# Performance work log

Measured on AMD Instinct MI355X. Metric: run time of the kernel, lower is better.

The kernel has to match this reference:

```python
import jax, jax.numpy as jnp
import numpy as np

RESO = 32          # grid_resolution
HID = 32           # hidden_dim
CDIM = 32          # c_dim
NBLK = 5           # n_blocks
PAD = 0.1          # padding
L = 10             # positional encoding frequencies -> dim 60


def setup_inputs() -> dict:
    key = jax.random.key(0)
    ks = jax.random.split(key, 12)
    B, T = 2, 200000
    p = jax.random.uniform(ks[0], (B, T, 3), jnp.float32, -0.5, 0.5)
    s = 0.05
    return {
        "p": p,
        "fc_pos_w": jax.random.normal(ks[1], (60, 2 * HID), jnp.float32) * s,
        "fc_pos_b": jax.random.normal(ks[2], (2 * HID,), jnp.float32) * s,
        "blk_fc0_w": jax.random.normal(ks[3], (NBLK, 2 * HID, HID), jnp.float32) * s,
        "blk_fc0_b": jax.random.normal(ks[4], (NBLK, HID), jnp.float32) * s,
        "blk_fc1_w": jax.random.normal(ks[5], (NBLK, HID, HID), jnp.float32) * s,
        "blk_fc1_b": jax.random.normal(ks[6], (NBLK, HID), jnp.float32) * s,
        "blk_sc_w": jax.random.normal(ks[7], (NBLK, 2 * HID, HID), jnp.float32) * s,  # shortcut, no bias
        "fc_c_w": jax.random.normal(ks[8], (HID, CDIM), jnp.float32) * s,
        "fc_c_b": jax.random.normal(ks[9], (CDIM,), jnp.float32) * s,
    }


def _pos_encode(p):
    # p in [-0.5,0.5] -> [-2,0] after 2p-1 (matches torch impl: p = 2*p - 1)
    q = 2.0 * p - 1.0
    freqs = (jnp.pi * (2.0 ** jnp.arange(L, dtype=jnp.float32)))  # [L]
    a = q[..., None, :] * freqs[:, None]                          # [B,T,L,3]
    pe = jnp.stack([jnp.sin(a), jnp.cos(a)], axis=-2)             # [B,T,L,2,3]
    return pe.reshape(*p.shape[:-1], 2 * L * 3)                   # [B,T,60]


def _normalize_3d(p):
    p_nor = p / (1.0 + PAD + 1e-3) + 0.5
    return jnp.clip(p_nor, 0.0, 1.0 - 1e-3)


def _coord2index(p_nor):
    x = jnp.floor(p_nor * RESO).astype(jnp.int32)                  # [B,T,3]
    return x[..., 0] + RESO * (x[..., 1] + RESO * x[..., 2])       # [B,T]


def _resblock(x, w0, b0, w1, b1, ws):
    h = jax.nn.relu(jax.nn.relu(x) @ w0 + b0)
    return x @ ws + (jax.nn.relu(h) @ w1 + b1)


def reference(p, fc_pos_w, fc_pos_b, blk_fc0_w, blk_fc0_b, blk_fc1_w, blk_fc1_b,
              blk_sc_w, fc_c_w, fc_c_b):
    B, T, _ = p.shape
    G = RESO ** 3
    p_nor = _normalize_3d(p)
    idx = _coord2index(p_nor)                                      # [B,T]
    gidx = (idx + jnp.arange(B, dtype=jnp.int32)[:, None] * G).reshape(-1)  # [B*T]

    net = _pos_encode(p) @ fc_pos_w + fc_pos_b                     # [B,T,64]
    net = _resblock(net, blk_fc0_w[0], blk_fc0_b[0], blk_fc1_w[0], blk_fc1_b[0], blk_sc_w[0])
    for i in range(1, NBLK):
        # pool_local: scatter_max per grid cell, gather back to points
        flat = net.reshape(B * T, HID)
        cell = jax.ops.segment_max(flat, gidx, num_segments=B * G)  # [B*G,HID]
        pooled = cell[gidx].reshape(B, T, HID)
        net = jnp.concatenate([net, pooled], axis=-1)               # [B,T,64]
        net = _resblock(net, blk_fc0_w[i], blk_fc0_b[i], blk_fc1_w[i], blk_fc1_b[i], blk_sc_w[i])

    c = net @ fc_c_w + fc_c_b                                       # [B,T,CDIM]

    # generate_grid_features: scatter_mean into grid (empty cells = 0)
    cf = c.reshape(B * T, CDIM)
    sums = jax.ops.segment_sum(cf, gidx, num_segments=B * G)        # [B*G,CDIM]
    cnt = jax.ops.segment_sum(jnp.ones((B * T, 1), c.dtype), gidx, num_segments=B * G)
    mean = sums / jnp.maximum(cnt, 1.0)
    fea_grid = mean.reshape(B, G, CDIM).transpose(0, 2, 1).reshape(B, CDIM, RESO, RESO, RESO)
    return fea_grid
```

## Files before the change

### kernel.cpp

```cpp
#include <hip/hip_runtime.h>
#include <math.h>

#define TPTS 200000
#define BB 2
#define NPTS (BB*TPTS)
#define GRID3 32768
#define BG 65536
#define SROWS 176

typedef __attribute__((ext_vector_type(8))) __bf16 bf16x8;
typedef __attribute__((ext_vector_type(4))) float f32x4;
typedef unsigned short ushort_t;

#define MFMA16(a,b,c) __builtin_amdgcn_mfma_f32_16x16x32_bf16(a,b,c,0,0,0)

__device__ __forceinline__ void split8(const float* v, bf16x8& hi, bf16x8& lo)
{
#pragma unroll
  for (int j = 0; j < 8; j++) {
    float f = v[j];
    __bf16 h = (__bf16)f;
    hi[j] = h;
    lo[j] = (__bf16)(f - (float)h);
  }
}

__device__ __forceinline__ int cellof(float p0, float p1, float p2, int t)
{
  const float DEN = (float)(1.0 + 0.1 + 1e-3);
  const float HI  = (float)(1.0 - 1e-3);
  float n0 = fminf(fmaxf(p0/DEN + 0.5f, 0.f), HI);
  float n1 = fminf(fmaxf(p1/DEN + 0.5f, 0.f), HI);
  float n2 = fminf(fmaxf(p2/DEN + 0.5f, 0.f), HI);
  int c0 = (int)floorf(n0*32.f), c1 = (int)floorf(n1*32.f), c2 = (int)floorf(n2*32.f);
  return c0 + 32*(c1 + 32*c2) + (t >= TPTS ? GRID3 : 0);
}

__global__ __launch_bounds__(256) void k_hist(
    const float* __restrict__ p, int* __restrict__ gbuf, int* __restrict__ hist)
{
  int t = blockIdx.x*256 + threadIdx.x;
  if (t >= NPTS) return;
  int g = cellof(p[3*t], p[3*t+1], p[3*t+2], t);
  gbuf[t] = g;
  atomicAdd(hist + g, 1);
}

__global__ __launch_bounds__(256) void k_scanA(
    const int* __restrict__ hist, int* __restrict__ texcl, int* __restrict__ bsum)
{
  __shared__ int sm[256];
  int tid = threadIdx.x;
  int t = blockIdx.x*256 + tid;
  int v = hist[t];
  sm[tid] = v; __syncthreads();
  for (int off = 1; off < 256; off <<= 1) {
    int x = sm[tid];
    int u = (tid >= off) ? sm[tid-off] : 0;
    __syncthreads();
    sm[tid] = x + u;
    __syncthreads();
  }
  texcl[t] = sm[tid] - v;
  if (tid == 255) bsum[blockIdx.x] = sm[255];
}

__global__ __launch_bounds__(256) void k_scanB(
    const int* __restrict__ bsum, int* __restrict__ boff)
{
  __shared__ int sm[256];
  int tid = threadIdx.x;
  int v = bsum[tid];
  sm[tid] = v; __syncthreads();
  for (int off = 1; off < 256; off <<= 1) {
    int x = sm[tid];
    int u = (tid >= off) ? sm[tid-off] : 0;
    __syncthreads();
    sm[tid] = x + u;
    __syncthreads();
  }
  boff[tid] = sm[tid] - v;
}

__global__ __launch_bounds__(256) void k_scanC(
    const int* __restrict__ texcl, const int* __restrict__ boff,
    int* __restrict__ start, int* __restrict__ cursor)
{
  int t = blockIdx.x*256 + threadIdx.x;
  int v = boff[blockIdx.x] + texcl[t];
  start[t] = v; cursor[t] = v;
  if (t == 0) start[BG] = NPTS;
}

__global__ __launch_bounds__(256) void k_scatter(
    const float* __restrict__ p, const int* __restrict__ gbuf,
    int* __restrict__ cursor, float* __restrict__ p_sorted, int* __restrict__ gsort)
{
  int t = blockIdx.x*256 + threadIdx.x;
  if (t >= NPTS) return;
  int g = gbuf[t];
  int slot = atomicAdd(cursor + g, 1);
  gsort[slot] = g;
  p_sorted[3*slot]   = p[3*t];
  p_sorted[3*slot+1] = p[3*t+1];
  p_sorted[3*slot+2] = p[3*t+2];
}

__global__ void k_pack(
    const float* __restrict__ f0w, const float* __restrict__ scw,
    const float* __restrict__ f1w, const float* __restrict__ wc,
    const float* __restrict__ Wp,
    ushort_t* __restrict__ wpack)
{
  int f = blockIdx.x, l = threadIdx.x;
  if (f >= 104) {
    int idx = f - 104;
    int c = idx >> 3, t = (idx >> 1) & 3, e = idx & 1;
#pragma unroll
    for (int j = 0; j < 8; j++) {
      int k = c*32 + (l>>4)*8 + j, n = t*16 + (l&15);
      float v = (k < 60) ? Wp[k*64 + n] : 0.f;
      __bf16 h = (__bf16)v;
      __bf16 out = (e == 0) ? h : (__bf16)(v - (float)h);
      union { __bf16 b; ushort_t u; } cv; cv.b = out;
      wpack[((size_t)f*64 + l)*8 + j] = cv.u;
    }
    return;
  }
  const float* W; int c, t, e;
  if (f < 100) {
    int s = f / 20, r = f % 20;
    if (r < 8)       { W = f0w + s*2048; c = r>>2;        t = (r>>1)&1; e = r&1; }
    else if (r < 16) { int q = r-8;  W = scw + s*2048; c = q>>2; t = (q>>1)&1; e = q&1; }
    else             { int q = r-16; W = f1w + s*1024; c = 0;    t = q>>1;     e = q&1; }
  } else { int q = f-100; W = wc; c = 0; t = q>>1; e = q&1; }
#pragma unroll
  for (int j = 0; j < 8; j++) {
    int k = c*32 + (l>>4)*8 + j, n = t*16 + (l&15);
    float v = W[k*32 + n];
    __bf16 h = (__bf16)v;
    __bf16 out = (e == 0) ? h : (__bf16)(v - (float)h);
    union { __bf16 b; ushort_t u; } cv; cv.b = out;
    wpack[((size_t)f*64 + l)*8 + j] = cv.u;
  }
}

__global__ __launch_bounds__(256) void k_fused0(
    const float* __restrict__ ps,
    const ushort_t* __restrict__ wpPE, const float* __restrict__ bp,
    const ushort_t* __restrict__ wp,
    const float* __restrict__ b0, const float* __restrict__ b1,
    float* __restrict__ net)
{
  __shared__ float xlds[4][16*68];
  __shared__ float hbuf[4][16*36];
  int wave = threadIdx.x >> 6, lane = threadIdx.x & 63;
  int m = lane & 15, q = lane >> 4;
  int pbase = (blockIdx.x*4 + wave)*16;
  int pt = pbase + m;

  float p0 = ps[3*pt], p1 = ps[3*pt+1], p2 = ps[3*pt+2];
  float u0 = 2.f*p0 - 1.f, u1 = 2.f*p1 - 1.f, u2 = 2.f*p2 - 1.f;
  const float PIF = 3.14159265358979323846f;

  float pe[2][8];
#pragma unroll
  for (int c2 = 0; c2 < 2; c2++) {
#pragma unroll
    for (int jj = 0; jj < 8; jj++) {
      int e = c2*32 + q*8 + jj;
      int l = (e * 43691) >> 18;
      int r = e - l*6;
      bool issin = (r < 3);
      int d = issin ? r : (r - 3);
      float ud = (d == 0) ? u0 : ((d == 1) ? u1 : u2);
      float xval = ldexpf(ud, l);
      float red = xval - 2.f*rintf(0.5f*xval);
      float ang = PIF*red + (issin ? 0.f : 1.5707963267948966f);
      float v = __sinf(ang);
      pe[c2][jj] = (e < 60) ? v : 0.f;
    }
  }
  bf16x8 peh[2], pel[2];
  split8(pe[0], peh[0], pel[0]);
  split8(pe[1], peh[1], pel[1]);

  f32x4 xacc[4];
#pragma unroll
  for (int t = 0; t < 4; t++) {
    float bb = bp[t*16 + m];
    xacc[t] = (f32x4){bb,bb,bb,bb};
  }
#pragma unroll
  for (int c2 = 0; c2 < 2; c2++)
#pragma unroll
    for (int t = 0; t < 4; t++) {
      bf16x8 bh = *(const bf16x8*)(wpPE + ((size_t)((c2*4+t)*2    )*64 + lane)*8);
      bf16x8 bl = *(const bf16x8*)(wpPE + ((size_t)((c2*4+t)*2 + 1)*64 + lane)*8);
      xacc[t] = MFMA16(peh[c2], bh, xacc[t]);
      xacc[t] = MFMA16(pel[c2], bh, xacc[t]);
      xacc[t] = MFMA16(peh[c2], bl, xacc[t]);
    }

  float* xl = xlds[wave];
#pragma unroll
  for (int t = 0; t < 4; t++)
#pragma unroll
    for (int r = 0; r < 4; r++)
      xl[(q*4+r)*68 + t*16 + m] = xacc[t][r];
  __syncthreads();

  float xv[2][8];
#pragma unroll
  for (int c2 = 0; c2 < 2; c2++)
#pragma unroll
    for (int jj = 0; jj < 8; jj++)
      xv[c2][jj] = xl[m*68 + c2*32 + q*8 + jj];

  bf16x8 w0f[2][2][2], wsf[2][2][2], w1f[2][2];
#pragma unroll
  for (int c = 0; c < 2; c++)
#pragma unroll
    for (int t = 0; t < 2; t++)
#pragma unroll
      for (int e = 0; e < 2; e++) {
        w0f[c][t][e] = *(const bf16x8*)(wp + ((size_t)(((c*2+t)*2+e)    )*64 + lane)*8);
        wsf[c][t][e] = *(const bf16x8*)(wp + ((size_t)(((c*2+t)*2+e) + 8)*64 + lane)*8);
      }
#pragma unroll
  for (int t = 0; t < 2; t++)
#pragma unroll
    for (int e = 0; e < 2; e++)
      w1f[t][e] = *(const bf16x8*)(wp + ((size_t)(16 + t*2 + e)*64 + lane)*8);

  bf16x8 axh[2], axl[2], arh[2], arl[2];
#pragma unroll
  for (int c = 0; c < 2; c++) {
    float r[8];
#pragma unroll
    for (int j = 0; j < 8; j++) r[j] = fmaxf(xv[c][j], 0.f);
    split8(xv[c], axh[c], axl[c]);
    split8(r,     arh[c], arl[c]);
  }

  f32x4 hacc[2], yacc[2];
#pragma unroll
  for (int t = 0; t < 2; t++) {
    float bb0 = b0[m + 16*t], bb1 = b1[m + 16*t];
    hacc[t] = (f32x4){bb0,bb0,bb0,bb0};
    yacc[t] = (f32x4){bb1,bb1,bb1,bb1};
  }

#pragma unroll
  for (int c = 0; c < 2; c++)
#pragma unroll
    for (int t = 0; t < 2; t++) {
      hacc[t] = MFMA16(arh[c], w0f[c][t][0], hacc[t]);
      hacc[t] = MFMA16(arl[c], w0f[c][t][0], hacc[t]);
      hacc[t] = MFMA16(arh[c], w0f[c][t][1], hacc[t]);
      yacc[t] = MFMA16(axh[c], wsf[c][t][0], yacc[t]);
      yacc[t] = MFMA16(axl[c], wsf[c][t][0], yacc[t]);
      yacc[t] = MFMA16(axh[c], wsf[c][t][1], yacc[t]);
    }

  float* hb = hbuf[wave];
#pragma unroll
  for (int t = 0; t < 2; t++)
#pragma unroll
    for (int r = 0; r < 4; r++)
      hb[(q*4+r)*36 + m + 16*t] = fmaxf(hacc[t][r], 0.f);
  __syncthreads();
  float hv[8];
#pragma unroll
  for (int j = 0; j < 8; j++) hv[j] = hb[m*36 + q*8 + j];
  bf16x8 hh, hl; split8(hv, hh, hl);
#pragma unroll
  for (int t = 0; t < 2; t++) {
    yacc[t] = MFMA16(hh, w1f[t][0], yacc[t]);
    yacc[t] = MFMA16(hl, w1f[t][0], yacc[t]);
    yacc[t] = MFMA16(hh, w1f[t][1], yacc[t]);
  }

#pragma unroll
  for (int t = 0; t < 2; t++)
#pragma unroll
    for (int r = 0; r < 4; r++)
      net[(size_t)(pbase + q*4 + r)*32 + m + 16*t] = yacc[t][r];
}

__global__ __launch_bounds__(256) void k_stage_f(
    const float* __restrict__ netin, float* __restrict__ netout,
    const int* __restrict__ gsort, const int* __restrict__ start,
    const ushort_t* __restrict__ wp,
    const float* __restrict__ b0, const float* __restrict__ b1)
{
  __shared__ float sbuf[SROWS*36];
  int tid = threadIdx.x;
  int P0 = blockIdx.x*64;
  int s = start[gsort[P0]];
  int e = start[gsort[P0+63] + 1];
  int n = e - s; if (n > SROWS) n = SROWS;

  for (int idx = tid; idx < n*8; idx += 256) {
    int r = idx >> 3, c = idx & 7;
    *(f32x4*)(sbuf + r*36 + c*4) =
      *(const f32x4*)(netin + ((size_t)(s + r))*32 + c*4);
  }
  __syncthreads();

  int wave = tid >> 6, lane = tid & 63;
  int m = lane & 15, q = lane >> 4;
  int pbase = P0 + wave*16;
  int pt = pbase + m;
  int g = gsort[pt];
  int cs = start[g] - s, ce = start[g+1] - s;

  float xv[2][8];
  {
    const float* xr = sbuf + (pt - s)*36 + q*8;
    *(f32x4*)&xv[0][0] = *(const f32x4*)xr;
    *(f32x4*)&xv[0][4] = *(const f32x4*)(xr + 4);
  }
  {
    f32x4 ma = (f32x4){-INFINITY,-INFINITY,-INFINITY,-INFINITY};
    f32x4 mb = ma;
    for (int k = cs; k < ce; k++) {
      const float* rr = sbuf + k*36 + q*8;
      f32x4 va = *(const f32x4*)rr;
      f32x4 vb = *(const f32x4*)(rr + 4);
      ma.x = fmaxf(ma.x, va.x); ma.y = fmaxf(ma.y, va.y);
      ma.z = fmaxf(ma.z, va.z); ma.w = fmaxf(ma.w, va.w);
      mb.x = fmaxf(mb.x, vb.x); mb.y = fmaxf(mb.y, vb.y);
      mb.z = fmaxf(mb.z, vb.z); mb.w = fmaxf(mb.w, vb.w);
    }
    *(f32x4*)&xv[1][0] = ma;
    *(f32x4*)&xv[1][4] = mb;
  }

  bf16x8 w0f[2][2][2], wsf[2][2][2], w1f[2][2];
#pragma unroll
  for (int c = 0; c < 2; c++)
#pragma unroll
    for (int t = 0; t < 2; t++)
#pragma unroll
      for (int e2 = 0; e2 < 2; e2++) {
        w0f[c][t][e2] = *(const bf16x8*)(wp + ((size_t)(((c*2+t)*2+e2)    )*64 + lane)*8);
        wsf[c][t][e2] = *(const bf16x8*)(wp + ((size_t)(((c*2+t)*2+e2) + 8)*64 + lane)*8);
      }
#pragma unroll
  for (int t = 0; t < 2; t++)
#pragma unroll
    for (int e2 = 0; e2 < 2; e2++)
      w1f[t][e2] = *(const bf16x8*)(wp + ((size_t)(16 + t*2 + e2)*64 + lane)*8);

  bf16x8 axh[2], axl[2], arh[2], arl[2];
#pragma unroll
  for (int c = 0; c < 2; c++) {
    float r[8];
#pragma unroll
    for (int j = 0; j < 8; j++) r[j] = fmaxf(xv[c][j], 0.f);
    split8(xv[c], axh[c], axl[c]);
    split8(r,     arh[c], arl[c]);
  }

  f32x4 hacc[2], yacc[2];
#pragma unroll
  for (int t = 0; t < 2; t++) {
    float bb0 = b0[m + 16*t], bb1 = b1[m + 16*t];
    hacc[t] = (f32x4){bb0,bb0,bb0,bb0};
    yacc[t] = (f32x4){bb1,bb1,bb1,bb1};
  }

#pragma unroll
  for (int c = 0; c < 2; c++)
#pragma unroll
    for (int t = 0; t < 2; t++) {
      hacc[t] = MFMA16(arh[c], w0f[c][t][0], hacc[t]);
      hacc[t] = MFMA16(arl[c], w0f[c][t][0], hacc[t]);
      hacc[t] = MFMA16(arh[c], w0f[c][t][1], hacc[t]);
      yacc[t] = MFMA16(axh[c], wsf[c][t][0], yacc[t]);
      yacc[t] = MFMA16(axl[c], wsf[c][t][0], yacc[t]);
      yacc[t] = MFMA16(axh[c], wsf[c][t][1], yacc[t]);
    }

  __syncthreads();
  float* hb = sbuf + wave*576;
#pragma unroll
  for (int t = 0; t < 2; t++)
#pragma unroll
    for (int r = 0; r < 4; r++)
      hb[(q*4+r)*36 + m + 16*t] = fmaxf(hacc[t][r], 0.f);
  __syncthreads();
  float hv[8];
#pragma unroll
  for (int j = 0; j < 8; j++) hv[j] = hb[m*36 + q*8 + j];
  bf16x8 hh, hl; split8(hv, hh, hl);
#pragma unroll
  for (int t = 0; t < 2; t++) {
    yacc[t] = MFMA16(hh, w1f[t][0], yacc[t]);
    yacc[t] = MFMA16(hl, w1f[t][0], yacc[t]);
    yacc[t] = MFMA16(hh, w1f[t][1], yacc[t]);
  }

#pragma unroll
  for (int t = 0; t < 2; t++)
#pragma unroll
    for (int r = 0; r < 4; r++)
      netout[(size_t)(pbase + q*4 + r)*32 + m + 16*t] = yacc[t][r];
}

__global__ __launch_bounds__(256) void k_final_f(
    const float* __restrict__ netin, float* __restrict__ netout,
    const int* __restrict__ gsort, const int* __restrict__ start,
    const ushort_t* __restrict__ wp, const ushort_t* __restrict__ wpc,
    const float* __restrict__ b0, const float* __restrict__ b1,
    const float* __restrict__ bc)
{
  __shared__ float sbuf[SROWS*36];
  int tid = threadIdx.x;
  int P0 = blockIdx.x*64;
  int s = start[gsort[P0]];
  int e = start[gsort[P0+63] + 1];
  int n = e - s; if (n > SROWS) n = SROWS;

  for (int idx = tid; idx < n*8; idx += 256) {
    int r = idx >> 3, c = idx & 7;
    *(f32x4*)(sbuf + r*36 + c*4) =
      *(const f32x4*)(netin + ((size_t)(s + r))*32 + c*4);
  }
  __syncthreads();

  int wave = tid >> 6, lane = tid & 63;
  int m = lane & 15, q = lane >> 4;
  int pbase = P0 + wave*16;
  int pt = pbase + m;
  int g = gsort[pt];
  int cs = start[g] - s, ce = start[g+1] - s;

  float xv[2][8];
  {
    const float* xr = sbuf + (pt - s)*36 + q*8;
    *(f32x4*)&xv[0][0] = *(const f32x4*)xr;
    *(f32x4*)&xv[0][4] = *(const f32x4*)(xr + 4);
  }
  {
    f32x4 ma = (f32x4){-INFINITY,-INFINITY,-INFINITY,-INFINITY};
    f32x4 mb = ma;
    for (int k = cs; k < ce; k++) {
      const float* rr = sbuf + k*36 + q*8;
      f32x4 va = *(const f32x4*)rr;
      f32x4 vb = *(const f32x4*)(rr + 4);
      ma.x = fmaxf(ma.x, va.x); ma.y = fmaxf(ma.y, va.y);
      ma.z = fmaxf(ma.z, va.z); ma.w = fmaxf(ma.w, va.w);
      mb.x = fmaxf(mb.x, vb.x); mb.y = fmaxf(mb.y, vb.y);
      mb.z = fmaxf(mb.z, vb.z); mb.w = fmaxf(mb.w, vb.w);
    }
    *(f32x4*)&xv[1][0] = ma;
    *(f32x4*)&xv[1][4] = mb;
  }

  bf16x8 w0f[2][2][2], wsf[2][2][2], w1f[2][2], wcf[2][2];
#pragma unroll
  for (int c = 0; c < 2; c++)
#pragma unroll
    for (int t = 0; t < 2; t++)
#pragma unroll
      for (int e2 = 0; e2 < 2; e2++) {
        w0f[c][t][e2] = *(const bf16x8*)(wp + ((size_t)(((c*2+t)*2+e2)    )*64 + lane)*8);
        wsf[c][t][e2] = *(const bf16x8*)(wp + ((size_t)(((c*2+t)*2+e2) + 8)*64 + lane)*8);
      }
#pragma unroll
  for (int t = 0; t < 2; t++)
#pragma unroll
    for (int e2 = 0; e2 < 2; e2++) {
      w1f[t][e2] = *(const bf16x8*)(wp  + ((size_t)(16 + t*2 + e2)*64 + lane)*8);
      wcf[t][e2] = *(const bf16x8*)(wpc + ((size_t)(     t*2 + e2)*64 + lane)*8);
    }

  bf16x8 axh[2], axl[2], arh[2], arl[2];
#pragma unroll
  for (int c = 0; c < 2; c++) {
    float r[8];
#pragma unroll
    for (int j = 0; j < 8; j++) r[j] = fmaxf(xv[c][j], 0.f);
    split8(xv[c], axh[c], axl[c]);
    split8(r,     arh[c], arl[c]);
  }

  f32x4 hacc[2], yacc[2];
#pragma unroll
  for (int t = 0; t < 2; t++) {
    float bb0 = b0[m + 16*t], bb1 = b1[m + 16*t];
    hacc[t] = (f32x4){bb0,bb0,bb0,bb0};
    yacc[t] = (f32x4){bb1,bb1,bb1,bb1};
  }

#pragma unroll
  for (int c = 0; c < 2; c++)
#pragma unroll
    for (int t = 0; t < 2; t++) {
      hacc[t] = MFMA16(arh[c], w0f[c][t][0], hacc[t]);
      hacc[t] = MFMA16(arl[c], w0f[c][t][0], hacc[t]);
      hacc[t] = MFMA16(arh[c], w0f[c][t][1], hacc[t]);
      yacc[t] = MFMA16(axh[c], wsf[c][t][0], yacc[t]);
      yacc[t] = MFMA16(axl[c], wsf[c][t][0], yacc[t]);
      yacc[t] = MFMA16(axh[c], wsf[c][t][1], yacc[t]);
    }

  __syncthreads();
  float* hb = sbuf + wave*576;
  float* yb = sbuf + 4*576 + wave*576;
#pragma unroll
  for (int t = 0; t < 2; t++)
#pragma unroll
    for (int r = 0; r < 4; r++)
      hb[(q*4+r)*36 + m + 16*t] = fmaxf(hacc[t][r], 0.f);
  __syncthreads();
  float hv[8];
#pragma unroll
  for (int j = 0; j < 8; j++) hv[j] = hb[m*36 + q*8 + j];
  bf16x8 hh, hl; split8(hv, hh, hl);
#pragma unroll
  for (int t = 0; t < 2; t++) {
    yacc[t] = MFMA16(hh, w1f[t][0], yacc[t]);
    yacc[t] = MFMA16(hl, w1f[t][0], yacc[t]);
    yacc[t] = MFMA16(hh, w1f[t][1], yacc[t]);
  }

#pragma unroll
  for (int t = 0; t < 2; t++)
#pragma unroll
    for (int r = 0; r < 4; r++)
      yb[(q*4+r)*36 + m + 16*t] = yacc[t][r];
  __syncthreads();
  float yv[8];
#pragma unroll
  for (int j = 0; j < 8; j++) yv[j] = yb[m*36 + q*8 + j];
  bf16x8 yh, yl; split8(yv, yh, yl);

  f32x4 cacc[2];
#pragma unroll
  for (int t = 0; t < 2; t++) {
    float bb = bc[m + 16*t];
    cacc[t] = (f32x4){bb,bb,bb,bb};
    cacc[t] = MFMA16(yh, wcf[t][0], cacc[t]);
    cacc[t] = MFMA16(yl, wcf[t][0], cacc[t]);
    cacc[t] = MFMA16(yh, wcf[t][1], cacc[t]);
  }

#pragma unroll
  for (int t = 0; t < 2; t++)
#pragma unroll
    for (int r = 0; r < 4; r++)
      netout[(size_t)(pbase + q*4 + r)*32 + m + 16*t] = cacc[t][r];
}

__global__ __launch_bounds__(256) void k_mean(
    const float* __restrict__ net, const int* __restrict__ start,
    float* __restrict__ outp)
{
  int tid = blockIdx.x*256 + threadIdx.x;
  int c = tid >> 3, sub = tid & 7;
  int s = start[c], e = start[c+1];
  f32x4 sum = (f32x4){0.f,0.f,0.f,0.f};
  for (int k = s; k < e; k++) {
    f32x4 v = *(const f32x4*)(net + (size_t)k*32 + sub*4);
    sum.x += v.x; sum.y += v.y; sum.z += v.z; sum.w += v.w;
  }
  float inv = (e > s) ? 1.f/(float)(e - s) : 0.f;
  int b = c >> 15, cell = c & 32767;
  size_t ob = ((size_t)b << 20) + cell;
#pragma unroll
  for (int jj = 0; jj < 4; jj++) {
    int ch = sub*4 + jj;
    float v = ((const float*)&sum)[jj] * inv;
    outp[ob + ((size_t)ch << 15)] = v;
  }
}

extern "C" void kernel_launch(void* const* d_in, const int* in_sizes, int n_in,
                              void* d_out, int out_size, void* d_ws, size_t ws_size,
                              hipStream_t stream)
{
  const float* p   = (const float*)d_in[0];
  const float* Wp  = (const float*)d_in[1];
  const float* bp  = (const float*)d_in[2];
  const float* f0w = (const float*)d_in[3];
  const float* f0b = (const float*)d_in[4];
  const float* f1w = (const float*)d_in[5];
  const float* f1b = (const float*)d_in[6];
  const float* scw = (const float*)d_in[7];
  const float* wc  = (const float*)d_in[8];
  const float* bc  = (const float*)d_in[9];
  float* outp = (float*)d_out;

  char* wsb = (char*)d_ws;
  float*    netA     = (float*)wsb;
  float*    netB     = netA + (size_t)NPTS*32;
  int*      gbuf     = (int*)(netB + (size_t)NPTS*32);
  int*      gsort    = gbuf + NPTS;
  int*      hist     = gsort + NPTS;
  int*      start    = hist + BG;
  int*      cursor   = start + BG + 1;
  int*      texcl    = cursor + BG;
  int*      bsum     = texcl + BG;
  int*      boff     = bsum + 256;
  ushort_t* wpack    = (ushort_t*)(boff + 256);
  float*    p_sorted = (float*)(wpack + (size_t)120*512);

  dim3 blk(256);
  dim3 gpts((NPTS + 255)/256);
  dim3 gmfma(NPTS/64);
  dim3 gcell((BG*8)/256);
  dim3 gscan(BG/256);

  hipMemsetAsync(hist, 0, (size_t)BG*4, stream);
  hipLaunchKernelGGL(k_hist, gpts, blk, 0, stream, p, gbuf, hist);
  hipLaunchKernelGGL(k_scanA, gscan, blk, 0, stream, hist, texcl, bsum);
  hipLaunchKernelGGL(k_scanB, dim3(1), blk, 0, stream, bsum, boff);
  hipLaunchKernelGGL(k_scanC, gscan, blk, 0, stream, texcl, boff, start, cursor);
  hipLaunchKernelGGL(k_scatter, gpts, blk, 0, stream, p, gbuf, cursor, p_sorted, gsort);
  hipLaunchKernelGGL(k_pack, dim3(120), dim3(64), 0, stream, f0w, scw, f1w, wc, Wp, wpack);
  hipLaunchKernelGGL(k_fused0, gmfma, blk, 0, stream,
                     p_sorted, wpack + (size_t)104*512, bp,
                     wpack + (size_t)0*20*512, f0b + 0*32, f1b + 0*32, netA);
  hipLaunchKernelGGL(k_stage_f, gmfma, blk, 0, stream, netA, netB, gsort, start,
                     wpack + (size_t)1*20*512, f0b + 1*32, f1b + 1*32);
  hipLaunchKernelGGL(k_stage_f, gmfma, blk, 0, stream, netB, netA, gsort, start,
                     wpack + (size_t)2*20*512, f0b + 2*32, f1b + 2*32);
  hipLaunchKernelGGL(k_stage_f, gmfma, blk, 0, stream, netA, netB, gsort, start,
                     wpack + (size_t)3*20*512, f0b + 3*32, f1b + 3*32);
  hipLaunchKernelGGL(k_final_f, gmfma, blk, 0, stream, netB, netA, gsort, start,
                     wpack + (size_t)4*20*512, wpack + (size_t)100*512,
                     f0b + 4*32, f1b + 4*32, bc);
  hipLaunchKernelGGL(k_mean, gcell, blk, 0, stream, netA, start, outp);
}
```

Measured before the change: 328.0 us.

## Fuse all resblock stages and scatter-mean into one cell-aligned megakernel

Replaces the per-stage kernels (fused0, three stage kernels, final, mean) with a single kernel. Each block owns a cell-aligned range of sorted points, found by binary search in a new k_blocks kernel, and keeps all activations in LDS across the five resblocks. The per-cell mean is written directly from LDS, so the global netA/netB round trips and several launches go away. The costs are an output memset, more __syncthreads, a 128-row cap per block that could drop points if a range is larger, and blocks with uneven work.

```diff
diff --git a/kernel.cpp b/kernel.cpp
--- a/kernel.cpp
+++ b/kernel.cpp
@@ -6,7 +6,7 @@
 #define NPTS (BB*TPTS)
 #define GRID3 32768
 #define BG 65536
-#define SROWS 176
+#define NMEGA (NPTS/64)
 
 typedef __attribute__((ext_vector_type(8))) __bf16 bf16x8;
 typedef __attribute__((ext_vector_type(4))) float f32x4;
@@ -106,6 +106,17 @@
   p_sorted[3*slot+2] = p[3*t+2];
 }
 
+__global__ __launch_bounds__(256) void k_blocks(
+    const int* __restrict__ start, int* __restrict__ blockA)
+{
+  int k = blockIdx.x*256 + threadIdx.x;
+  if (k > NMEGA) return;
+  int t = k*64;
+  int lo = 0, hi = BG;
+  while (lo < hi) { int mid = (lo+hi) >> 1; if (start[mid] >= t) hi = mid; else lo = mid+1; }
+  blockA[k] = start[lo];
+}
+
 __global__ void k_pack(
     const float* __restrict__ f0w, const float* __restrict__ scw,
     const float* __restrict__ f1w, const float* __restrict__ wc,
@@ -145,436 +156,333 @@
   }
 }
 
-__global__ __launch_bounds__(256) void k_fused0(
-    const float* __restrict__ ps,
-    const ushort_t* __restrict__ wpPE, const float* __restrict__ bp,
-    const ushort_t* __restrict__ wp,
-    const float* __restrict__ b0, const float* __restrict__ b1,
-    float* __restrict__ net)
-{
-  __shared__ float xlds[4][16*68];
-  __shared__ float hbuf[4][16*36];
-  int wave = threadIdx.x >> 6, lane = threadIdx.x & 63;
-  int m = lane & 15, q = lane >> 4;
-  int pbase = (blockIdx.x*4 + wave)*16;
-  int pt = pbase + m;
-
-  float p0 = ps[3*pt], p1 = ps[3*pt+1], p2 = ps[3*pt+2];
-  float u0 = 2.f*p0 - 1.f, u1 = 2.f*p1 - 1.f, u2 = 2.f*p2 - 1.f;
-  const float PIF = 3.14159265358979323846f;
-
-  float pe[2][8];
-#pragma unroll
-  for (int c2 = 0; c2 < 2; c2++) {
-#pragma unroll
-    for (int jj = 0; jj < 8; jj++) {
-      int e = c2*32 + q*8 + jj;
-      int l = (e * 43691) >> 18;
-      int r = e - l*6;
-      bool issin = (r < 3);
-      int d = issin ? r : (r - 3);
-      float ud = (d == 0) ? u0 : ((d == 1) ? u1 : u2);
-      float xval = ldexpf(ud, l);
-      float red = xval - 2.f*rintf(0.5f*xval);
-      float ang = PIF*red + (issin ? 0.f : 1.5707963267948966f);
-      float v = __sinf(ang);
-      pe[c2][jj] = (e < 60) ? v : 0.f;
-    }
-  }
-  bf16x8 peh[2], pel[2];
-  split8(pe[0], peh[0], pel[0]);
-  split8(pe[1], peh[1], pel[1]);
-
-  f32x4 xacc[4];
-#pragma unroll
-  for (int t = 0; t < 4; t++) {
-    float bb = bp[t*16 + m];
-    xacc[t] = (f32x4){bb,bb,bb,bb};
-  }
-#pragma unroll
-  for (int c2 = 0; c2 < 2; c2++)
-#pragma unroll
-    for (int t = 0; t < 4; t++) {
-      bf16x8 bh = *(const bf16x8*)(wpPE + ((size_t)((c2*4+t)*2    )*64 + lane)*8);
-      bf16x8 bl = *(const bf16x8*)(wpPE + ((size_t)((c2*4+t)*2 + 1)*64 + lane)*8);
-      xacc[t] = MFMA16(peh[c2], bh, xacc[t]);
-      xacc[t] = MFMA16(pel[c2], bh, xacc[t]);
-      xacc[t] = MFMA16(peh[c2], bl, xacc[t]);
-    }
-
-  float* xl = xlds[wave];
-#pragma unroll
-  for (int t = 0; t < 4; t++)
-#pragma unroll
-    for (int r = 0; r < 4; r++)
-      xl[(q*4+r)*68 + t*16 + m] = xacc[t][r];
-  __syncthreads();
-
-  float xv[2][8];
-#pragma unroll
-  for (int c2 = 0; c2 < 2; c2++)
-#pragma unroll
-    for (int jj = 0; jj < 8; jj++)
-      xv[c2][jj] = xl[m*68 + c2*32 + q*8 + jj];
-
-  bf16x8 w0f[2][2][2], wsf[2][2][2], w1f[2][2];
-#pragma unroll
-  for (int c = 0; c < 2; c++)
-#pragma unroll
-    for (int t = 0; t < 2; t++)
-#pragma unroll
-      for (int e = 0; e < 2; e++) {
-        w0f[c][t][e] = *(const bf16x8*)(wp + ((size_t)(((c*2+t)*2+e)    )*64 + lane)*8);
-        wsf[c][t][e] = *(const bf16x8*)(wp + ((size_t)(((c*2+t)*2+e) + 8)*64 + lane)*8);
-      }
-#pragma unroll
-  for (int t = 0; t < 2; t++)
-#pragma unroll
-    for (int e = 0; e < 2; e++)
-      w1f[t][e] = *(const bf16x8*)(wp + ((size_t)(16 + t*2 + e)*64 + lane)*8);
-
-  bf16x8 axh[2], axl[2], arh[2], arl[2];
-#pragma unroll
-  for (int c = 0; c < 2; c++) {
-    float r[8];
-#pragma unroll
-    for (int j = 0; j < 8; j++) r[j] = fmaxf(xv[c][j], 0.f);
-    split8(xv[c], axh[c], axl[c]);
-    split8(r,     arh[c], arl[c]);
-  }
-
-  f32x4 hacc[2], yacc[2];
-#pragma unroll
-  for (int t = 0; t < 2; t++) {
-    float bb0 = b0[m + 16*t], bb1 = b1[m + 16*t];
-    hacc[t] = (f32x4){bb0,bb0,bb0,bb0};
-    yacc[t] = (f32x4){bb1,bb1,bb1,bb1};
-  }
-
-#pragma unroll
-  for (int c = 0; c < 2; c++)
-#pragma unroll
-    for (int t = 0; t < 2; t++) {
-      hacc[t] = MFMA16(arh[c], w0f[c][t][0], hacc[t]);
-      hacc[t] = MFMA16(arl[c], w0f[c][t][0], hacc[t]);
-      hacc[t] = MFMA16(arh[c], w0f[c][t][1], hacc[t]);
-      yacc[t] = MFMA16(axh[c], wsf[c][t][0], yacc[t]);
-      yacc[t] = MFMA16(axl[c], wsf[c][t][0], yacc[t]);
-      yacc[t] = MFMA16(axh[c], wsf[c][t][1], yacc[t]);
-    }
-
-  float* hb = hbuf[wave];
-#pragma unroll
-  for (int t = 0; t < 2; t++)
-#pragma unroll
-    for (int r = 0; r < 4; r++)
-      hb[(q*4+r)*36 + m + 16*t] = fmaxf(hacc[t][r], 0.f);
-  __syncthreads();
-  float hv[8];
-#pragma unroll
-  for (int j = 0; j < 8; j++) hv[j] = hb[m*36 + q*8 + j];
-  bf16x8 hh, hl; split8(hv, hh, hl);
-#pragma unroll
-  for (int t = 0; t < 2; t++) {
-    yacc[t] = MFMA16(hh, w1f[t][0], yacc[t]);
-    yacc[t] = MFMA16(hl, w1f[t][0], yacc[t]);
-    yacc[t] = MFMA16(hh, w1f[t][1], yacc[t]);
-  }
-
-#pragma unroll
-  for (int t = 0; t < 2; t++)
-#pragma unroll
-    for (int r = 0; r < 4; r++)
-      net[(size_t)(pbase + q*4 + r)*32 + m + 16*t] = yacc[t][r];
-}
-
-__global__ __launch_bounds__(256) void k_stage_f(
-    const float* __restrict__ netin, float* __restrict__ netout,
-    const int* __restrict__ gsort, const int* __restrict__ start,
-    const ushort_t* __restrict__ wp,
-    const float* __restrict__ b0, const float* __restrict__ b1)
-{
-  __shared__ float sbuf[SROWS*36];
+__global__ __launch_bounds__(256) void k_mega(
+    const float* __restrict__ ps, const int* __restrict__ gsort,
+    const int* __restrict__ start, const int* __restrict__ blockA,
+    const ushort_t* __restrict__ wpack,
+    const float* __restrict__ bp, const float* __restrict__ f0b,
+    const float* __restrict__ f1b, const float* __restrict__ bc,
+    float* __restrict__ outp)
+{
+  __shared__ __align__(16) float smem[4608*2 + 4*576];
+  float* actA = smem;
+  float* actB = smem + 4608;
+  float* hbB  = smem + 9216;
+
   int tid = threadIdx.x;
-  int P0 = blockIdx.x*64;
-  int s = start[gsort[P0]];
-  int e = start[gsort[P0+63] + 1];
-  int n = e - s; if (n > SROWS) n = SROWS;
-
-  for (int idx = tid; idx < n*8; idx += 256) {
-    int r = idx >> 3, c = idx & 7;
-    *(f32x4*)(sbuf + r*36 + c*4) =
-      *(const f32x4*)(netin + ((size_t)(s + r))*32 + c*4);
-  }
-  __syncthreads();
+  int s = blockA[blockIdx.x], e = blockA[blockIdx.x + 1];
+  int n = e - s;
+  if (n <= 0) return;
+  if (n > 128) n = 128;
 
   int wave = tid >> 6, lane = tid & 63;
   int m = lane & 15, q = lane >> 4;
-  int pbase = P0 + wave*16;
-  int pt = pbase + m;
-  int g = gsort[pt];
-  int cs = start[g] - s, ce = start[g+1] - s;
-
-  float xv[2][8];
+  float* hb = hbB + wave*576;
+  const float PIF = 3.14159265358979323846f;
+
+  int ptc[2], rown[2], cs[2], ce[2];
+#pragma unroll
+  for (int c = 0; c < 2; c++) {
+    int pt = s + c*64 + wave*16 + m;
+    int pc = pt < e ? pt : (e-1);
+    ptc[c] = pc; rown[c] = pc - s;
+    int g = gsort[pc];
+    cs[c] = start[g] - s; ce[c] = start[g+1] - s;
+  }
+
   {
-    const float* xr = sbuf + (pt - s)*36 + q*8;
-    *(f32x4*)&xv[0][0] = *(const f32x4*)xr;
-    *(f32x4*)&xv[0][4] = *(const f32x4*)(xr + 4);
-  }
-  {
-    f32x4 ma = (f32x4){-INFINITY,-INFINITY,-INFINITY,-INFINITY};
-    f32x4 mb = ma;
-    for (int k = cs; k < ce; k++) {
-      const float* rr = sbuf + k*36 + q*8;
-      f32x4 va = *(const f32x4*)rr;
-      f32x4 vb = *(const f32x4*)(rr + 4);
-      ma.x = fmaxf(ma.x, va.x); ma.y = fmaxf(ma.y, va.y);
-      ma.z = fmaxf(ma.z, va.z); ma.w = fmaxf(ma.w, va.w);
-      mb.x = fmaxf(mb.x, vb.x); mb.y = fmaxf(mb.y, vb.y);
-      mb.z = fmaxf(mb.z, vb.z); mb.w = fmaxf(mb.w, vb.w);
+    const ushort_t* wp0 = wpack;
+    const ushort_t* wpPE = wpack + (size_t)104*512;
+    bf16x8 w0f[2][2][2], wsf[2][2][2], w1f[2][2];
+#pragma unroll
+    for (int c = 0; c < 2; c++)
+#pragma unroll
+      for (int t = 0; t < 2; t++)
+#pragma unroll
+        for (int e2 = 0; e2 < 2; e2++) {
+          w0f[c][t][e2] = *(const bf16x8*)(wp0 + ((size_t)(((c*2+t)*2+e2)    )*64 + lane)*8);
+          wsf[c][t][e2] = *(const bf16x8*)(wp0 + ((size_t)(((c*2+t)*2+e2) + 8)*64 + lane)*8);
+        }
+#pragma unroll
+    for (int t = 0; t < 2; t++)
+#pragma unroll
+      for (int e2 = 0; e2 < 2; e2++)
+        w1f[t][e2] = *(const bf16x8*)(wp0 + ((size_t)(16 + t*2 + e2)*64 + lane)*8);
+
+#pragma unroll
+    for (int c = 0; c < 2; c++) {
+      if (c*64 >= n) continue;
+      int pc = ptc[c];
+      float p0 = ps[3*pc], p1 = ps[3*pc+1], p2 = ps[3*pc+2];
+      float u0 = 2.f*p0 - 1.f, u1 = 2.f*p1 - 1.f, u2 = 2.f*p2 - 1.f;
+      float pe[2][8];
+#pragma unroll
+      for (int c2 = 0; c2 < 2; c2++)
+#pragma unroll
+        for (int jj = 0; jj < 8; jj++) {
+          int e1 = c2*32 + q*8 + jj;
+          int l = (e1 * 43691) >> 18;
+          int r = e1 - l*6;
+          bool issin = (r < 3);
+          int d = issin ? r : (r - 3);
+          float ud = (d == 0) ? u0 : ((d == 1) ? u1 : u2);
+          float xval = ldexpf(ud, l);
+          float red = xval - 2.f*rintf(0.5f*xval);
+          float sv, cv;
+          __sincosf(PIF*red, &sv, &cv);
+          float v = issin ? sv : cv;
+          pe[c2][jj] = (e1 < 60) ? v : 0.f;
+        }
+      bf16x8 peh[2], pel[2];
+      split8(pe[0], peh[0], pel[0]);
+      split8(pe[1], peh[1], pel[1]);
+
+      f32x4 xacc[4];
+#pragma unroll
+      for (int t = 0; t < 4; t++) {
+        float bb = bp[t*16 + m];
+        xacc[t] = (f32x4){bb,bb,bb,bb};
+      }
+#pragma unroll
+      for (int c2 = 0; c2 < 2; c2++)
+#pragma unroll
+        for (int t = 0; t < 4; t++) {
+          bf16x8 bh = *(const bf16x8*)(wpPE + ((size_t)((c2*4+t)*2    )*64 + lane)*8);
+          bf16x8 bl = *(const bf16x8*)(wpPE + ((size_t)((c2*4+t)*2 + 1)*64 + lane)*8);
+          xacc[t] = MFMA16(peh[c2], bh, xacc[t]);
+          xacc[t] = MFMA16(pel[c2], bh, xacc[t]);
+          xacc[t] = MFMA16(peh[c2], bl, xacc[t]);
+        }
+
+      float* xl = actB + wave*1088;
+#pragma unroll
+      for (int t = 0; t < 4; t++)
+#pragma unroll
+        for (int r = 0; r < 4; r++)
+          xl[(q*4+r)*68 + t*16 + m] = xacc[t][r];
+      __syncthreads();
+      float xv[2][8];
+#pragma unroll
+      for (int c2 = 0; c2 < 2; c2++)
+#pragma unroll
+        for (int jj = 0; jj < 8; jj++)
+          xv[c2][jj] = xl[m*68 + c2*32 + q*8 + jj];
+      __syncthreads();
+
+      bf16x8 axh[2], axl[2], arh[2], arl[2];
+#pragma unroll
+      for (int c2 = 0; c2 < 2; c2++) {
+        float r[8];
+#pragma unroll
+        for (int j = 0; j < 8; j++) r[j] = fmaxf(xv[c2][j], 0.f);
+        split8(xv[c2], axh[c2], axl[c2]);
+        split8(r,      arh[c2], arl[c2]);
+      }
+      f32x4 hacc[2], yacc[2];
+#pragma unroll
+      for (int t = 0; t < 2; t++) {
+        float bb0 = f0b[m + 16*t], bb1 = f1b[m + 16*t];
+        hacc[t] = (f32x4){bb0,bb0,bb0,bb0};
+        yacc[t] = (f32x4){bb1,bb1,bb1,bb1};
+      }
+#pragma unroll
+      for (int c2 = 0; c2 < 2; c2++)
+#pragma unroll
+        for (int t = 0; t < 2; t++) {
+          hacc[t] = MFMA16(arh[c2], w0f[c2][t][0], hacc[t]);
+          hacc[t] = MFMA16(arl[c2], w0f[c2][t][0], hacc[t]);
+          hacc[t] = MFMA16(arh[c2], w0f[c2][t][1], hacc[t]);
+          yacc[t] = MFMA16(axh[c2], wsf[c2][t][0], yacc[t]);
+          yacc[t] = MFMA16(axl[c2], wsf[c2][t][0], yacc[t]);
+          yacc[t] = MFMA16(axh[c2], wsf[c2][t][1], yacc[t]);
+        }
+#pragma unroll
+      for (int t = 0; t < 2; t++)
+#pragma unroll
+        for (int r = 0; r < 4; r++)
+          hb[(q*4+r)*36 + m + 16*t] = fmaxf(hacc[t][r], 0.f);
+      __syncthreads();
+      float hv[8];
+#pragma unroll
+      for (int j = 0; j < 8; j++) hv[j] = hb[m*36 + q*8 + j];
+      __syncthreads();
+      bf16x8 hh, hl; split8(hv, hh, hl);
+#pragma unroll
+      for (int t = 0; t < 2; t++) {
+        yacc[t] = MFMA16(hh, w1f[t][0], yacc[t]);
+        yacc[t] = MFMA16(hl, w1f[t][0], yacc[t]);
+        yacc[t] = MFMA16(hh, w1f[t][1], yacc[t]);
+      }
+#pragma unroll
+      for (int t = 0; t < 2; t++)
+#pragma unroll
+        for (int r = 0; r < 4; r++) {
+          int prow = c*64 + wave*16 + q*4 + r;
+          if (prow < n) actA[prow*36 + m + 16*t] = yacc[t][r];
+        }
+      __syncthreads();
     }
-    *(f32x4*)&xv[1][0] = ma;
-    *(f32x4*)&xv[1][4] = mb;
-  }
-
-  bf16x8 w0f[2][2][2], wsf[2][2][2], w1f[2][2];
-#pragma unroll
-  for (int c = 0; c < 2; c++)
+  }
+  __syncthreads();
+
+  for (int st = 1; st <= 4; st++) {
+    const float* bin = (st & 1) ? actA : actB;
+    float* bout = (st & 1) ? actB : actA;
+    bool last = (st == 4);
+    const ushort_t* wp = wpack + (size_t)st*20*512;
+    const float* b0 = f0b + st*32;
+    const float* b1 = f1b + st*32;
+
+    bf16x8 w0f[2][2][2], wsf[2][2][2], w1f[2][2], wcf[2][2];
+#pragma unroll
+    for (int c = 0; c < 2; c++)
+#pragma unroll
+      for (int t = 0; t < 2; t++)
+#pragma unroll
+        for (int e2 = 0; e2 < 2; e2++) {
+          w0f[c][t][e2] = *(const bf16x8*)(wp + ((size_t)(((c*2+t)*2+e2)    )*64 + lane)*8);
+          wsf[c][t][e2] = *(const bf16x8*)(wp + ((size_t)(((c*2+t)*2+e2) + 8)*64 + lane)*8);
+        }
 #pragma unroll
     for (int t = 0; t < 2; t++)
 #pragma unroll
       for (int e2 = 0; e2 < 2; e2++) {
-        w0f[c][t][e2] = *(const bf16x8*)(wp + ((size_t)(((c*2+t)*2+e2)    )*64 + lane)*8);
-        wsf[c][t][e2] = *(const bf16x8*)(wp + ((size_t)(((c*2+t)*2+e2) + 8)*64 + lane)*8);
-      }
-#pragma unroll
-  for (int t = 0; t < 2; t++)
-#pragma unroll
-    for (int e2 = 0; e2 < 2; e2++)
-      w1f[t][e2] = *(const bf16x8*)(wp + ((size_t)(16 + t*2 + e2)*64 + lane)*8);
-
-  bf16x8 axh[2], axl[2], arh[2], arl[2];
-#pragma unroll
-  for (int c = 0; c < 2; c++) {
-    float r[8];
-#pragma unroll
-    for (int j = 0; j < 8; j++) r[j] = fmaxf(xv[c][j], 0.f);
-    split8(xv[c], axh[c], axl[c]);
-    split8(r,     arh[c], arl[c]);
-  }
-
-  f32x4 hacc[2], yacc[2];
-#pragma unroll
-  for (int t = 0; t < 2; t++) {
-    float bb0 = b0[m + 16*t], bb1 = b1[m + 16*t];
-    hacc[t] = (f32x4){bb0,bb0,bb0,bb0};
-    yacc[t] = (f32x4){bb1,bb1,bb1,bb1};
-  }
-
-#pragma unroll
-  for (int c = 0; c < 2; c++)
-#pragma unroll
-    for (int t = 0; t < 2; t++) {
-      hacc[t] = MFMA16(arh[c], w0f[c][t][0], hacc[t]);
-      hacc[t] = MFMA16(arl[c], w0f[c][t][0], hacc[t]);
-      hacc[t] = MFMA16(arh[c], w0f[c][t][1], hacc[t]);
-      yacc[t] = MFMA16(axh[c], wsf[c][t][0], yacc[t]);
-      yacc[t] = MFMA16(axl[c], wsf[c][t][0], yacc[t]);
-      yacc[t] = MFMA16(axh[c], wsf[c][t][1], yacc[t]);
+        w1f[t][e2] = *(const bf16x8*)(wp + ((size_t)(16 + t*2 + e2)*64 + lane)*8);
+        wcf[t][e2] = *(const bf16x8*)(wpack + ((size_t)(100 + t*2 + e2)*64 + lane)*8);
+      }
+
+#pragma unroll
+    for (int c = 0; c < 2; c++) {
+      if (c*64 >= n) continue;
+      float xv[2][8];
+      {
+        const float* xr = bin + rown[c]*36 + q*8;
+        *(f32x4*)&xv[0][0] = *(const f32x4*)xr;
+        *(f32x4*)&xv[0][4] = *(const f32x4*)(xr + 4);
+      }
+      {
+        f32x4 ma = (f32x4){-INFINITY,-INFINITY,-INFINITY,-INFINITY};
+        f32x4 mb = ma;
+        for (int k = cs[c]; k < ce[c]; k++) {
+          const float* rr = bin + k*36 + q*8;
+          f32x4 va = *(const f32x4*)rr;
+          f32x4 vb = *(const f32x4*)(rr + 4);
+          ma.x = fmaxf(ma.x, va.x); ma.y = fmaxf(ma.y, va.y);
+          ma.z = fmaxf(ma.z, va.z); ma.w = fmaxf(ma.w, va.w);
+          mb.x = fmaxf(mb.x, vb.x); mb.y = fmaxf(mb.y, vb.y);
+          mb.z = fmaxf(mb.z, vb.z); mb.w = fmaxf(mb.w, vb.w);
+        }
+        *(f32x4*)&xv[1][0] = ma;
+        *(f32x4*)&xv[1][4] = mb;
+      }
+
+      bf16x8 axh[2], axl[2], arh[2], arl[2];
+#pragma unroll
+      for (int c2 = 0; c2 < 2; c2++) {
+        float r[8];
+#pragma unroll
+        for (int j = 0; j < 8; j++) r[j] = fmaxf(xv[c2][j], 0.f);
+        split8(xv[c2], axh[c2], axl[c2]);
+        split8(r,      arh[c2], arl[c2]);
+      }
+      f32x4 hacc[2], yacc[2];
+#pragma unroll
+      for (int t = 0; t < 2; t++) {
+        float bb0 = b0[m + 16*t], bb1 = b1[m + 16*t];
+        hacc[t] = (f32x4){bb0,bb0,bb0,bb0};
+        yacc[t] = (f32x4){bb1,bb1,bb1,bb1};
+      }
+#pragma unroll
+      for (int c2 = 0; c2 < 2; c2++)
+#pragma unroll
+        for (int t = 0; t < 2; t++) {
+          hacc[t] = MFMA16(arh[c2], w0f[c2][t][0], hacc[t]);
+          hacc[t] = MFMA16(arl[c2], w0f[c2][t][0], hacc[t]);
+          hacc[t] = MFMA16(arh[c2], w0f[c2][t][1], hacc[t]);
+          yacc[t] = MFMA16(axh[c2], wsf[c2][t][0], yacc[t]);
+          yacc[t] = MFMA16(axl[c2], wsf[c2][t][0], yacc[t]);
+          yacc[t] = MFMA16(axh[c2], wsf[c2][t][1], yacc[t]);
+        }
+#pragma unroll
+      for (int t = 0; t < 2; t++)
+#pragma unroll
+        for (int r = 0; r < 4; r++)
+          hb[(q*4+r)*36 + m + 16*t] = fmaxf(hacc[t][r], 0.f);
+      __syncthreads();
+      float hv[8];
+#pragma unroll
+      for (int j = 0; j < 8; j++) hv[j] = hb[m*36 + q*8 + j];
+      __syncthreads();
+      bf16x8 hh, hl; split8(hv, hh, hl);
+#pragma unroll
+      for (int t = 0; t < 2; t++) {
+        yacc[t] = MFMA16(hh, w1f[t][0], yacc[t]);
+        yacc[t] = MFMA16(hl, w1f[t][0], yacc[t]);
+        yacc[t] = MFMA16(hh, w1f[t][1], yacc[t]);
+      }
+
+      if (!last) {
+#pragma unroll
+        for (int t = 0; t < 2; t++)
+#pragma unroll
+          for (int r = 0; r < 4; r++) {
+            int prow = c*64 + wave*16 + q*4 + r;
+            if (prow < n) bout[prow*36 + m + 16*t] = yacc[t][r];
+          }
+      } else {
+#pragma unroll
+        for (int t = 0; t < 2; t++)
+#pragma unroll
+          for (int r = 0; r < 4; r++)
+            hb[(q*4+r)*36 + m + 16*t] = yacc[t][r];
+        __syncthreads();
+        float yv[8];
+#pragma unroll
+        for (int j = 0; j < 8; j++) yv[j] = hb[m*36 + q*8 + j];
+        __syncthreads();
+        bf16x8 yh, yl; split8(yv, yh, yl);
+        f32x4 cacc[2];
+#pragma unroll
+        for (int t = 0; t < 2; t++) {
+          float bb = bc[m + 16*t];
+          cacc[t] = (f32x4){bb,bb,bb,bb};
+          cacc[t] = MFMA16(yh, wcf[t][0], cacc[t]);
+          cacc[t] = MFMA16(yl, wcf[t][0], cacc[t]);
+          cacc[t] = MFMA16(yh, wcf[t][1], cacc[t]);
+        }
+#pragma unroll
+        for (int t = 0; t < 2; t++)
+#pragma unroll
+          for (int r = 0; r < 4; r++) {
+            int prow = c*64 + wave*16 + q*4 + r;
+            if (prow < n) bout[prow*36 + m + 16*t] = cacc[t][r];
+          }
+      }
+      __syncthreads();
     }
-
-  __syncthreads();
-  float* hb = sbuf + wave*576;
-#pragma unroll
-  for (int t = 0; t < 2; t++)
-#pragma unroll
-    for (int r = 0; r < 4; r++)
-      hb[(q*4+r)*36 + m + 16*t] = fmaxf(hacc[t][r], 0.f);
-  __syncthreads();
-  float hv[8];
-#pragma unroll
-  for (int j = 0; j < 8; j++) hv[j] = hb[m*36 + q*8 + j];
-  bf16x8 hh, hl; split8(hv, hh, hl);
-#pragma unroll
-  for (int t = 0; t < 2; t++) {
-    yacc[t] = MFMA16(hh, w1f[t][0], yacc[t]);
-    yacc[t] = MFMA16(hl, w1f[t][0], yacc[t]);
-    yacc[t] = MFMA16(hh, w1f[t][1], yacc[t]);
-  }
-
-#pragma unroll
-  for (int t = 0; t < 2; t++)
-#pragma unroll
-    for (int r = 0; r < 4; r++)
-      netout[(size_t)(pbase + q*4 + r)*32 + m + 16*t] = yacc[t][r];
-}
-
-__global__ __launch_bounds__(256) void k_final_f(
-    const float* __restrict__ netin, float* __restrict__ netout,
-    const int* __restrict__ gsort, const int* __restrict__ start,
-    const ushort_t* __restrict__ wp, const ushort_t* __restrict__ wpc,
-    const float* __restrict__ b0, const float* __restrict__ b1,
-    const float* __restrict__ bc)
-{
-  __shared__ float sbuf[SROWS*36];
-  int tid = threadIdx.x;
-  int P0 = blockIdx.x*64;
-  int s = start[gsort[P0]];
-  int e = start[gsort[P0+63] + 1];
-  int n = e - s; if (n > SROWS) n = SROWS;
-
-  for (int idx = tid; idx < n*8; idx += 256) {
-    int r = idx >> 3, c = idx & 7;
-    *(f32x4*)(sbuf + r*36 + c*4) =
-      *(const f32x4*)(netin + ((size_t)(s + r))*32 + c*4);
-  }
-  __syncthreads();
-
-  int wave = tid >> 6, lane = tid & 63;
-  int m = lane & 15, q = lane >> 4;
-  int pbase = P0 + wave*16;
-  int pt = pbase + m;
-  int g = gsort[pt];
-  int cs = start[g] - s, ce = start[g+1] - s;
-
-  float xv[2][8];
-  {
-    const float* xr = sbuf + (pt - s)*36 + q*8;
-    *(f32x4*)&xv[0][0] = *(const f32x4*)xr;
-    *(f32x4*)&xv[0][4] = *(const f32x4*)(xr + 4);
-  }
-  {
-    f32x4 ma = (f32x4){-INFINITY,-INFINITY,-INFINITY,-INFINITY};
-    f32x4 mb = ma;
-    for (int k = cs; k < ce; k++) {
-      const float* rr = sbuf + k*36 + q*8;
-      f32x4 va = *(const f32x4*)rr;
-      f32x4 vb = *(const f32x4*)(rr + 4);
-      ma.x = fmaxf(ma.x, va.x); ma.y = fmaxf(ma.y, va.y);
-      ma.z = fmaxf(ma.z, va.z); ma.w = fmaxf(ma.w, va.w);
-      mb.x = fmaxf(mb.x, vb.x); mb.y = fmaxf(mb.y, vb.y);
-      mb.z = fmaxf(mb.z, vb.z); mb.w = fmaxf(mb.w, vb.w);
+    __syncthreads();
+  }
+
+  for (int r = tid; r < n; r += 256) {
+    int pt = s + r;
+    int g = gsort[pt];
+    int gs = start[g];
+    if (gs != pt) continue;
+    int ge = start[g+1];
+    float inv = 1.f / (float)(ge - gs);
+    int b = g >> 15, cell = g & 32767;
+    size_t ob = ((size_t)b << 20) + cell;
+#pragma unroll
+    for (int sub = 0; sub < 8; sub++) {
+      f32x4 sm = (f32x4){0.f,0.f,0.f,0.f};
+      for (int rr = gs - s; rr < ge - s; rr++) {
+        f32x4 v = *(const f32x4*)(actA + rr*36 + sub*4);
+        sm.x += v.x; sm.y += v.y; sm.z += v.z; sm.w += v.w;
+      }
+#pragma unroll
+      for (int j = 0; j < 4; j++)
+        outp[ob + ((size_t)(sub*4 + j) << 15)] = ((float*)&sm)[j] * inv;
     }
-    *(f32x4*)&xv[1][0] = ma;
-    *(f32x4*)&xv[1][4] = mb;
-  }
-
-  bf16x8 w0f[2][2][2], wsf[2][2][2], w1f[2][2], wcf[2][2];
-#pragma unroll
-  for (int c = 0; c < 2; c++)
-#pragma unroll
-    for (int t = 0; t < 2; t++)
-#pragma unroll
-      for (int e2 = 0; e2 < 2; e2++) {
-        w0f[c][t][e2] = *(const bf16x8*)(wp + ((size_t)(((c*2+t)*2+e2)    )*64 + lane)*8);
-        wsf[c][t][e2] = *(const bf16x8*)(wp + ((size_t)(((c*2+t)*2+e2) + 8)*64 + lane)*8);
-      }
-#pragma unroll
-  for (int t = 0; t < 2; t++)
-#pragma unroll
-    for (int e2 = 0; e2 < 2; e2++) {
-      w1f[t][e2] = *(const bf16x8*)(wp  + ((size_t)(16 + t*2 + e2)*64 + lane)*8);
-      wcf[t][e2] = *(const bf16x8*)(wpc + ((size_t)(     t*2 + e2)*64 + lane)*8);
-    }
-
-  bf16x8 axh[2], axl[2], arh[2], arl[2];
-#pragma unroll
-  for (int c = 0; c < 2; c++) {
-    float r[8];
-#pragma unroll
-    for (int j = 0; j < 8; j++) r[j] = fmaxf(xv[c][j], 0.f);
-    split8(xv[c], axh[c], axl[c]);
-    split8(r,     arh[c], arl[c]);
-  }
-
-  f32x4 hacc[2], yacc[2];
-#pragma unroll
-  for (int t = 0; t < 2; t++) {
-    float bb0 = b0[m + 16*t], bb1 = b1[m + 16*t];
-    hacc[t] = (f32x4){bb0,bb0,bb0,bb0};
-    yacc[t] = (f32x4){bb1,bb1,bb1,bb1};
-  }
-
-#pragma unroll
-  for (int c = 0; c < 2; c++)
-#pragma unroll
-    for (int t = 0; t < 2; t++) {
-      hacc[t] = MFMA16(arh[c], w0f[c][t][0], hacc[t]);
-      hacc[t] = MFMA16(arl[c], w0f[c][t][0], hacc[t]);
-      hacc[t] = MFMA16(arh[c], w0f[c][t][1], hacc[t]);
-      yacc[t] = MFMA16(axh[c], wsf[c][t][0], yacc[t]);
-      yacc[t] = MFMA16(axl[c], wsf[c][t][0], yacc[t]);
-      yacc[t] = MFMA16(axh[c], wsf[c][t][1], yacc[t]);
-    }
-
-  __syncthreads();
-  float* hb = sbuf + wave*576;
-  float* yb = sbuf + 4*576 + wave*576;
-#pragma unroll
-  for (int t = 0; t < 2; t++)
-#pragma unroll
-    for (int r = 0; r < 4; r++)
-      hb[(q*4+r)*36 + m + 16*t] = fmaxf(hacc[t][r], 0.f);
-  __syncthreads();
-  float hv[8];
-#pragma unroll
-  for (int j = 0; j < 8; j++) hv[j] = hb[m*36 + q*8 + j];
-  bf16x8 hh, hl; split8(hv, hh, hl);
-#pragma unroll
-  for (int t = 0; t < 2; t++) {
-    yacc[t] = MFMA16(hh, w1f[t][0], yacc[t]);
-    yacc[t] = MFMA16(hl, w1f[t][0], yacc[t]);
-    yacc[t] = MFMA16(hh, w1f[t][1], yacc[t]);
-  }
-
-#pragma unroll
-  for (int t = 0; t < 2; t++)
-#pragma unroll
-    for (int r = 0; r < 4; r++)
-      yb[(q*4+r)*36 + m + 16*t] = yacc[t][r];
-  __syncthreads();
-  float yv[8];
-#pragma unroll
-  for (int j = 0; j < 8; j++) yv[j] = yb[m*36 + q*8 + j];
-  bf16x8 yh, yl; split8(yv, yh, yl);
-
-  f32x4 cacc[2];
-#pragma unroll
-  for (int t = 0; t < 2; t++) {
-    float bb = bc[m + 16*t];
-    cacc[t] = (f32x4){bb,bb,bb,bb};
-    cacc[t] = MFMA16(yh, wcf[t][0], cacc[t]);
-    cacc[t] = MFMA16(yl, wcf[t][0], cacc[t]);
-    cacc[t] = MFMA16(yh, wcf[t][1], cacc[t]);
-  }
-
-#pragma unroll
-  for (int t = 0; t < 2; t++)
-#pragma unroll
-    for (int r = 0; r < 4; r++)
-      netout[(size_t)(pbase + q*4 + r)*32 + m + 16*t] = cacc[t][r];
-}
-
-__global__ __launch_bounds__(256) void k_mean(
-    const float* __restrict__ net, const int* __restrict__ start,
-    float* __restrict__ outp)
-{
-  int tid = blockIdx.x*256 + threadIdx.x;
-  int c = tid >> 3, sub = tid & 7;
-  int s = start[c], e = start[c+1];
-  f32x4 sum = (f32x4){0.f,0.f,0.f,0.f};
-  for (int k = s; k < e; k++) {
-    f32x4 v = *(const f32x4*)(net + (size_t)k*32 + sub*4);
-    sum.x += v.x; sum.y += v.y; sum.z += v.z; sum.w += v.w;
-  }
-  float inv = (e > s) ? 1.f/(float)(e - s) : 0.f;
-  int b = c >> 15, cell = c & 32767;
-  size_t ob = ((size_t)b << 20) + cell;
-#pragma unroll
-  for (int jj = 0; jj < 4; jj++) {
-    int ch = sub*4 + jj;
-    float v = ((const float*)&sum)[jj] * inv;
-    outp[ob + ((size_t)ch << 15)] = v;
   }
 }
 
@@ -595,9 +503,7 @@
   float* outp = (float*)d_out;
 
   char* wsb = (char*)d_ws;
-  float*    netA     = (float*)wsb;
-  float*    netB     = netA + (size_t)NPTS*32;
-  int*      gbuf     = (int*)(netB + (size_t)NPTS*32);
+  int*      gbuf     = (int*)wsb;
   int*      gsort    = gbuf + NPTS;
   int*      hist     = gsort + NPTS;
   int*      start    = hist + BG;
@@ -605,33 +511,24 @@
   int*      texcl    = cursor + BG;
   int*      bsum     = texcl + BG;
   int*      boff     = bsum + 256;
-  ushort_t* wpack    = (ushort_t*)(boff + 256);
+  int*      blockA   = boff + 256;
+  ushort_t* wpack    = (ushort_t*)(blockA + NMEGA + 1);
   float*    p_sorted = (float*)(wpack + (size_t)120*512);
 
   dim3 blk(256);
   dim3 gpts((NPTS + 255)/256);
-  dim3 gmfma(NPTS/64);
-  dim3 gcell((BG*8)/256);
   dim3 gscan(BG/256);
 
   hipMemsetAsync(hist, 0, (size_t)BG*4, stream);
+  hipMemsetAsync(outp, 0, (size_t)out_size*sizeof(float), stream);
   hipLaunchKernelGGL(k_hist, gpts, blk, 0, stream, p, gbuf, hist);
   hipLaunchKernelGGL(k_scanA, gscan, blk, 0, stream, hist, texcl, bsum);
   hipLaunchKernelGGL(k_scanB, dim3(1), blk, 0, stream, bsum, boff);
   hipLaunchKernelGGL(k_scanC, gscan, blk, 0, stream, texcl, boff, start, cursor);
   hipLaunchKernelGGL(k_scatter, gpts, blk, 0, stream, p, gbuf, cursor, p_sorted, gsort);
+  hipLaunchKernelGGL(k_blocks, dim3((NMEGA + 256)/256), blk, 0, stream, start, blockA);
   hipLaunchKernelGGL(k_pack, dim3(120), dim3(64), 0, stream, f0w, scw, f1w, wc, Wp, wpack);
-  hipLaunchKernelGGL(k_fused0, gmfma, blk, 0, stream,
-                     p_sorted, wpack + (size_t)104*512, bp,
-                     wpack + (size_t)0*20*512, f0b + 0*32, f1b + 0*32, netA);
-  hipLaunchKernelGGL(k_stage_f, gmfma, blk, 0, stream, netA, netB, gsort, start,
-                     wpack + (size_t)1*20*512, f0b + 1*32, f1b + 1*32);
-  hipLaunchKernelGGL(k_stage_f, gmfma, blk, 0, stream, netB, netA, gsort, start,
-                     wpack + (size_t)2*20*512, f0b + 2*32, f1b + 2*32);
-  hipLaunchKernelGGL(k_stage_f, gmfma, blk, 0, stream, netA, netB, gsort, start,
-                     wpack + (size_t)3*20*512, f0b + 3*32, f1b + 3*32);
-  hipLaunchKernelGGL(k_final_f, gmfma, blk, 0, stream, netB, netA, gsort, start,
-                     wpack + (size_t)4*20*512, wpack + (size_t)100*512,
-                     f0b + 4*32, f1b + 4*32, bc);
-  hipLaunchKernelGGL(k_mean, gcell, blk, 0, stream, netA, start, outp);
-}
+  hipLaunchKernelGGL(k_mega, dim3(NMEGA), blk, 0, stream,
+                     p_sorted, gsort, start, blockA, wpack,
+                     bp, f0b, f1b, bc, outp);
+}
```

New measurement: 477.8 us. 1.46x slower.
